# Optimization experiments

Measured on AMD Instinct MI355X. Metric: run time of the kernel, lower is better.

The kernel has to match this reference:

```python
import jax, jax.numpy as jnp
import numpy as np

IMAGE_SIZE = 128
FACES_PER_PIXEL = 4
BLUR_RADIUS = 0.01
EPS = 1e-8


def setup_inputs() -> dict:
    key = jax.random.key(0)
    k1, k2, k3 = jax.random.split(key, 3)
    B, V, F = 2, 2000, 800
    # verts are already projected to screen/NDC space: x,y in [-1,1], z > 0 (depth)
    xy = jax.random.uniform(k1, (B, V, 2), minval=-1.0, maxval=1.0)
    z = jax.random.uniform(k2, (B, V, 1), minval=0.5, maxval=2.5)
    verts = jnp.concatenate([xy, z], axis=-1).astype(jnp.float32)
    faces = jax.random.randint(k3, (F, 3), 0, V)
    return {"verts": verts, "faces": faces}


def _edge(a, b, p):
    # signed parallelogram area of (a -> b -> p), using xy components only
    return (p[..., 0] - a[..., 0]) * (b[..., 1] - a[..., 1]) - (
        p[..., 1] - a[..., 1]) * (b[..., 0] - a[..., 0])


def _seg_dist2(p, a, b):
    # squared distance from point p to segment [a, b] in 2D
    ab = b - a
    pa = p - a
    t = jnp.clip(jnp.sum(pa * ab, -1) / (jnp.sum(ab * ab, -1) + EPS), 0.0, 1.0)
    d = pa - t[..., None] * ab
    return jnp.sum(d * d, -1)


def _rasterize(verts, faces):
    H = W = IMAGE_SIZE
    K = FACES_PER_PIXEL
    B = verts.shape[0]
    fv = verts[:, faces]                      # [B,F,3,3] gather face vertices
    v0, v1, v2 = fv[:, :, 0], fv[:, :, 1], fv[:, :, 2]
    a0 = v0[:, None, :, :2]                   # [B,1,F,2]
    a1 = v1[:, None, :, :2]
    a2 = v2[:, None, :, :2]
    z0 = v0[:, None, :, 2]                    # [B,1,F]
    z1 = v1[:, None, :, 2]
    z2 = v2[:, None, :, 2]
    # pixel centers in NDC, pytorch3d convention: index 0 -> +1, last -> -1
    xs = 1.0 - 2.0 * (jnp.arange(W, dtype=verts.dtype) + 0.5) / W
    ys = 1.0 - 2.0 * (jnp.arange(H, dtype=verts.dtype) + 0.5) / H
    yy, xx = jnp.meshgrid(ys, xs, indexing="ij")
    p = jnp.stack([xx, yy], -1).reshape(1, -1, 1, 2)   # [1,P,1,2], P=H*W

    area = _edge(a0, a1, a2)                  # [B,1,F] signed face area*2
    w0 = _edge(a1, a2, p)                     # [B,P,F]
    w1 = _edge(a2, a0, p)
    w2 = _edge(a0, a1, p)
    denom = jnp.where(jnp.abs(area) > EPS, area,
                      jnp.where(area >= 0, EPS, -EPS))
    b0, b1, b2 = w0 / denom, w1 / denom, w2 / denom
    zpix = b0 * z0 + b1 * z1 + b2 * z2        # [B,P,F] interpolated depth

    inside = (b0 >= 0) & (b1 >= 0) & (b2 >= 0)
    dmin = jnp.minimum(_seg_dist2(p, a0, a1),
                       jnp.minimum(_seg_dist2(p, a1, a2),
                                   _seg_dist2(p, a2, a0)))
    dsign = jnp.where(inside, -dmin, dmin)    # signed squared edge distance

    valid = (inside | (dmin < BLUR_RADIUS)) & (zpix > EPS) & (
        jnp.abs(area) > EPS)
    zcand = jnp.where(valid, zpix, jnp.inf)
    _, idx = jax.lax.top_k(-zcand, K)         # K nearest faces per pixel

    take = lambda x: jnp.take_along_axis(x, idx, axis=-1)
    sel_valid = take(valid)
    pix_to_face = jnp.where(sel_valid, idx, -1)
    zbuf = jnp.where(sel_valid, take(zpix), -1.0)
    bary = jnp.stack([b0, b1, b2], -1)        # [B,P,F,3]
    bsel = jnp.take_along_axis(bary, idx[..., None], axis=2)  # [B,P,K,3]
    bsel = jnp.where(sel_valid[..., None], bsel, -1.0)
    dsel = jnp.where(sel_valid, take(dsign), -1.0)

    return (pix_to_face.reshape(B, H, W, K),
            zbuf.reshape(B, H, W, K),
            bsel.reshape(B, H, W, K, 3),
            dsel.reshape(B, H, W, K))


def reference(verts, faces):
    # Fragments: (pix_to_face, zbuf, bary_coords, dists)
    return _rasterize(verts, faces)
```

## Files before the change

kernel.cpp:

```cpp
#include <hip/hip_runtime.h>

#define IMG   128
#define KF    4
#define NF    800
#define NV    2000
#define NB    2
#define EPSF  1e-8f
#define BLURF 0.01f
#define CULL_D2 0.0103f
#define HEXT    0.0547f

typedef unsigned long long u64;
#define INVK ((((u64)0x7f800000u) << 32) | 0xffffffffu)

#pragma clang fp contract(off)

__device__ __forceinline__ float rcp2(float d) {
    float y = __builtin_amdgcn_rcpf(d);
    float e = __builtin_fmaf(-d, y, 1.0f);
    y = __builtin_fmaf(y, e, y);
    e = __builtin_fmaf(-d, y, 1.0f);
    y = __builtin_fmaf(y, e, y);
    return y;
}
__device__ __forceinline__ float fdivr(float n, float d, float y) {
    float q0 = n * y;
    float r  = __builtin_fmaf(-d, q0, n);
    return __builtin_fmaf(r, y, q0);
}

__device__ __forceinline__ float seg_d2(float pax, float pay, float abx, float aby) {
#pragma clang fp contract(off)
    float dd = (abx * abx + aby * aby) + EPSF;
    float t  = (pax * abx + pay * aby) / dd;
    t = fminf(fmaxf(t, 0.0f), 1.0f);
    float dx = pax - t * abx;
    float dy = pay - t * aby;
    return dx * dx + dy * dy;
}

__device__ __forceinline__ float seg_d2f(float pax, float pay, float abx, float aby) {
#pragma clang fp contract(off)
    float dd = (abx * abx + aby * aby) + EPSF;
    float n  = pax * abx + pay * aby;
    float t  = fdivr(n, dd, rcp2(dd));
    t = fminf(fmaxf(t, 0.0f), 1.0f);
    float dx = pax - t * abx;
    float dy = pay - t * aby;
    return dx * dx + dy * dy;
}

__device__ __forceinline__ void ins4(u64& s0, u64& s1, u64& s2, u64& s3, u64 k) {
    bool c0 = k < s0, c1 = k < s1, c2 = k < s2, c3 = k < s3;
    s3 = c2 ? s2 : (c3 ? k : s3);
    s2 = c1 ? s1 : (c2 ? k : s2);
    s1 = c0 ? s0 : (c1 ? k : s1);
    s0 = c0 ? k  : s0;
}

__global__ __launch_bounds__(256) void raster_p1(
    const float* __restrict__ verts,
    const int*   __restrict__ faces,
    u64* __restrict__ ws,
    int sh)
{
#pragma clang fp contract(off)
    extern __shared__ char dynLDS[];
    __shared__ u64 sK[2 * 4 * 64];
    __shared__ int sTot;

    const int S     = 1 << sh;
    const int chunk = NF >> sh;
    float* sFD  = (float*)dynLDS;
    int*   sList = (int*)(dynLDS + (size_t)chunk * 10 * sizeof(float));

    const int tid   = threadIdx.x;
    const int blk   = blockIdx.x;
    const int tile  = blk >> sh;
    const int slice = blk & (S - 1);
    const int b     = tile >> 8;
    const int trow  = (tile & 255) >> 4;
    const int tcol  = tile & 15;
    const float* vb = verts + b * NV * 3;
    const int fbase = slice * chunk;

    if (tid == 0) sTot = 0;

    for (int j = tid; j < chunk; j += 256) {
        int f = fbase + j;
        int i0 = faces[3 * f + 0], i1 = faces[3 * f + 1], i2 = faces[3 * f + 2];
        float a0x = vb[3 * i0], a0y = vb[3 * i0 + 1], z0 = vb[3 * i0 + 2];
        float a1x = vb[3 * i1], a1y = vb[3 * i1 + 1], z1 = vb[3 * i1 + 2];
        float a2x = vb[3 * i2], a2y = vb[3 * i2 + 1], z2 = vb[3 * i2 + 2];
        float area = (a2x - a0x) * (a1y - a0y) - (a2y - a0y) * (a1x - a0x);
        float aab  = fabsf(area);
        float denom = (aab > EPSF) ? area : (area >= 0.0f ? EPSF : -EPSF);
        float* fd = &sFD[j * 10];
        fd[0] = a0x; fd[1] = a0y; fd[2] = a1x; fd[3] = a1y; fd[4] = a2x; fd[5] = a2y;
        fd[6] = z0;  fd[7] = z1;  fd[8] = z2;  fd[9] = denom;
    }
    __syncthreads();

    const int wave = tid >> 6;
    const int lane = tid & 63;
    const int pr = lane >> 3, pc = lane & 7;
    const int row = trow * 8 + pr, col = tcol * 8 + pc;
    const float px = 1.0f - (2.0f * ((float)col + 0.5f)) / 128.0f;
    const float py = 1.0f - (2.0f * ((float)row + 0.5f)) / 128.0f;
    const float txmax = 1.0f - (2.0f * ((float)(tcol * 8)     + 0.5f)) / 128.0f;
    const float txmin = 1.0f - (2.0f * ((float)(tcol * 8 + 7) + 0.5f)) / 128.0f;
    const float tymax = 1.0f - (2.0f * ((float)(trow * 8)     + 0.5f)) / 128.0f;
    const float tymin = 1.0f - (2.0f * ((float)(trow * 8 + 7) + 0.5f)) / 128.0f;
    const float cx = 0.5f * (txmin + txmax);
    const float cy = 0.5f * (tymin + tymax);

    for (int j = tid; j < chunk; j += 256) {
        const float* fd = &sFD[j * 10];
        float a0x = fd[0], a0y = fd[1], a1x = fd[2], a1y = fd[3], a2x = fd[4], a2y = fd[5];
        float area = (a2x - a0x) * (a1y - a0y) - (a2y - a0y) * (a1x - a0x);
        bool surv = fabsf(area) > EPSF;
        float bxmin = fminf(a0x, fminf(a1x, a2x)) - 0.101f;
        float bxmax = fmaxf(a0x, fmaxf(a1x, a2x)) + 0.101f;
        float bymin = fminf(a0y, fminf(a1y, a2y)) - 0.101f;
        float bymax = fmaxf(a0y, fmaxf(a1y, a2y)) + 0.101f;
        surv &= !(bxmin > txmax || bxmax < txmin || bymin > tymax || bymax < tymin);
        float s = (area >= 0.0f) ? 1.0f : -1.0f;
        float e0x = a2x - a1x, e0y = a2y - a1y;
        float e1x = a0x - a2x, e1y = a0y - a2y;
        float e2x = a1x - a0x, e2y = a1y - a0y;
        float w0 = s * ((cx - a1x) * e0y - (cy - a1y) * e0x) + HEXT * (fabsf(e0x) + fabsf(e0y));
        float w1 = s * ((cx - a2x) * e1y - (cy - a2y) * e1x) + HEXT * (fabsf(e1x) + fabsf(e1y));
        float w2 = s * ((cx - a0x) * e2y - (cy - a0y) * e2x) + HEXT * (fabsf(e2x) + fabsf(e2y));
        float l0 = e0x * e0x + e0y * e0y;
        float l1 = e1x * e1x + e1y * e1y;
        float l2 = e2x * e2x + e2y * e2y;
        surv &= !((w0 < 0.0f) & (w0 * w0 > CULL_D2 * l0));
        surv &= !((w1 < 0.0f) & (w1 * w1 > CULL_D2 * l1));
        surv &= !((w2 < 0.0f) & (w2 * w2 > CULL_D2 * l2));
        if (surv) {
            int pos = atomicAdd(&sTot, 1);
            sList[pos] = j;
        }
    }
    __syncthreads();
    const int total = sTot;

    u64 s0 = INVK, s1 = INVK, s2 = INVK, s3 = INVK;
    for (int j = wave; j < total; j += 4) {
        int lf = sList[j];
        const float* fd = &sFD[lf * 10];
        float a0x = fd[0], a0y = fd[1], a1x = fd[2], a1y = fd[3], a2x = fd[4], a2y = fd[5];
        float z0 = fd[6], z1 = fd[7], z2 = fd[8], denom = fd[9];
        float e0x = a2x - a1x, e0y = a2y - a1y;
        float e1x = a0x - a2x, e1y = a0y - a2y;
        float e2x = a1x - a0x, e2y = a1y - a0y;
        float p0x = px - a0x, p0y = py - a0y;
        float p1x = px - a1x, p1y = py - a1y;
        float p2x = px - a2x, p2y = py - a2y;
        float w0 = p1x * e0y - p1y * e0x;
        float w1 = p2x * e1y - p2y * e1x;
        float w2 = p0x * e2y - p0y * e2x;
        float yd = rcp2(denom);
        float b0 = fdivr(w0, denom, yd);
        float b1 = fdivr(w1, denom, yd);
        float b2 = fdivr(w2, denom, yd);
        float zpix = (b0 * z0 + b1 * z1) + b2 * z2;
        bool inside = fminf(b0, fminf(b1, b2)) >= 0.0f;
        bool valid;
        if (__all(inside)) {
            valid = (zpix > EPSF);
        } else {
            float dA = seg_d2f(p0x, p0y, e2x, e2y);
            float dB = seg_d2f(p1x, p1y, e0x, e0y);
            float dC = seg_d2f(p2x, p2y, e1x, e1y);
            float dmin = fminf(dA, fminf(dB, dC));
            valid = (inside | (dmin < BLURF)) & (zpix > EPSF);
        }
        u64 key = valid ? ((((u64)__float_as_uint(zpix)) << 32) | (unsigned)(fbase + lf)) : INVK;
        if (__any(key < s3)) ins4(s0, s1, s2, s3, key);
    }

    if (wave >= 2) {
        int r = wave - 2;
        sK[(r * 4 + 0) * 64 + lane] = s0;
        sK[(r * 4 + 1) * 64 + lane] = s1;
        sK[(r * 4 + 2) * 64 + lane] = s2;
        sK[(r * 4 + 3) * 64 + lane] = s3;
    }
    __syncthreads();
    if (wave < 2) {
        ins4(s0, s1, s2, s3, sK[(wave * 4 + 0) * 64 + lane]);
        ins4(s0, s1, s2, s3, sK[(wave * 4 + 1) * 64 + lane]);
        ins4(s0, s1, s2, s3, sK[(wave * 4 + 2) * 64 + lane]);
        ins4(s0, s1, s2, s3, sK[(wave * 4 + 3) * 64 + lane]);
    }
    __syncthreads();
    if (wave == 1) {
        sK[0 * 64 + lane] = s0;
        sK[1 * 64 + lane] = s1;
        sK[2 * 64 + lane] = s2;
        sK[3 * 64 + lane] = s3;
    }
    __syncthreads();
    if (wave == 0) {
        ins4(s0, s1, s2, s3, sK[0 * 64 + lane]);
        ins4(s0, s1, s2, s3, sK[1 * 64 + lane]);
        ins4(s0, s1, s2, s3, sK[2 * 64 + lane]);
        ins4(s0, s1, s2, s3, sK[3 * 64 + lane]);
        u64* wrow = ws + (size_t)blk * 256;
        wrow[0 * 64 + lane] = s0;
        wrow[1 * 64 + lane] = s1;
        wrow[2 * 64 + lane] = s2;
        wrow[3 * 64 + lane] = s3;
    }
}

__global__ __launch_bounds__(256) void raster_p2(
    const float* __restrict__ verts,
    const int*   __restrict__ faces,
    const u64* __restrict__ ws,
    int sh,
    float* __restrict__ out0, float* __restrict__ out1,
    float* __restrict__ out2, float* __restrict__ out3)
{
#pragma clang fp contract(off)
    __shared__ u64 sK[4 * 64];
    const int S    = 1 << sh;
    const int tid  = threadIdx.x;
    const int tile = blockIdx.x;
    const int b    = tile >> 8;
    const int trow = (tile & 255) >> 4;
    const int tcol = tile & 15;
    const float* vb = verts + b * NV * 3;

    if (tid < 64) {
        u64 s0 = INVK, s1 = INVK, s2 = INVK, s3 = INVK;
        const u64* base = ws + (size_t)tile * S * 256;
        for (int s = 0; s < S; ++s) {
            ins4(s0, s1, s2, s3, base[s * 256 + 0 * 64 + tid]);
            ins4(s0, s1, s2, s3, base[s * 256 + 1 * 64 + tid]);
            ins4(s0, s1, s2, s3, base[s * 256 + 2 * 64 + tid]);
            ins4(s0, s1, s2, s3, base[s * 256 + 3 * 64 + tid]);
        }
        sK[0 * 64 + tid] = s0;
        sK[1 * 64 + tid] = s1;
        sK[2 * 64 + tid] = s2;
        sK[3 * 64 + tid] = s3;
    }
    __syncthreads();

    int pix = tid >> 2, k = tid & 3;
    u64 key = sK[k * 64 + pix];
    int prow = pix >> 3, pcol = pix & 7;
    int grow = trow * 8 + prow, gcol = tcol * 8 + pcol;
    int p = (b * IMG + grow) * IMG + gcol;
    float qx = 1.0f - (2.0f * ((float)gcol + 0.5f)) / 128.0f;
    float qy = 1.0f - (2.0f * ((float)grow + 0.5f)) / 128.0f;
    float o0 = -1.0f, o1 = -1.0f, ob0 = -1.0f, ob1 = -1.0f, ob2 = -1.0f, o3 = -1.0f;
    if ((unsigned)(key >> 32) != 0x7f800000u) {
        int fi = (int)(unsigned)(key & 0xffffffffu);
        int i0 = faces[3 * fi + 0], i1 = faces[3 * fi + 1], i2 = faces[3 * fi + 2];
        float a0x = vb[3 * i0], a0y = vb[3 * i0 + 1], z0 = vb[3 * i0 + 2];
        float a1x = vb[3 * i1], a1y = vb[3 * i1 + 1], z1 = vb[3 * i1 + 2];
        float a2x = vb[3 * i2], a2y = vb[3 * i2 + 1], z2 = vb[3 * i2 + 2];
        float area = (a2x - a0x) * (a1y - a0y) - (a2y - a0y) * (a1x - a0x);
        float aab  = fabsf(area);
        float denom = (aab > EPSF) ? area : (area >= 0.0f ? EPSF : -EPSF);
        float e0x = a2x - a1x, e0y = a2y - a1y;
        float e1x = a0x - a2x, e1y = a0y - a2y;
        float e2x = a1x - a0x, e2y = a1y - a0y;
        float p0x = qx - a0x, p0y = qy - a0y;
        float p1x = qx - a1x, p1y = qy - a1y;
        float p2x = qx - a2x, p2y = qy - a2y;
        float w0 = p1x * e0y - p1y * e0x;
        float w1 = p2x * e1y - p2y * e1x;
        float w2 = p0x * e2y - p0y * e2x;
        float b0 = w0 / denom, b1 = w1 / denom, b2 = w2 / denom;
        float zpix = (b0 * z0 + b1 * z1) + b2 * z2;
        bool inside = (b0 >= 0.0f) & (b1 >= 0.0f) & (b2 >= 0.0f);
        float dA = seg_d2(p0x, p0y, e2x, e2y);
        float dB = seg_d2(p1x, p1y, e0x, e0y);
        float dC = seg_d2(p2x, p2y, e1x, e1y);
        float dmin = fminf(dA, fminf(dB, dC));
        o0 = (float)fi;
        o1 = zpix;
        ob0 = b0; ob1 = b1; ob2 = b2;
        o3 = inside ? -dmin : dmin;
    }
    int o = p * KF + k;
    out0[o] = o0;
    out1[o] = o1;
    out2[o * 3 + 0] = ob0;
    out2[o * 3 + 1] = ob1;
    out2[o * 3 + 2] = ob2;
    out3[o] = o3;
}

extern "C" void kernel_launch(void* const* d_in, const int* in_sizes, int n_in,
                              void* d_out, int out_size, void* d_ws, size_t ws_size,
                              hipStream_t stream) {
    const float* verts = (const float*)d_in[0];
    const int*   faces = (const int*)d_in[1];
    float* out = (float*)d_out;
    const int n0 = NB * IMG * IMG * KF;

    const size_t per_slice = 512ull * 256 * sizeof(u64);
    int sh;
    if      (ws_size >= 4 * per_slice) sh = 2;
    else if (ws_size >= 2 * per_slice) sh = 1;
    else                               sh = 0;
    const int S = 1 << sh;
    const int chunk = NF >> sh;
    const size_t dyn = (size_t)chunk * 10 * sizeof(float) + (size_t)chunk * sizeof(int);

    raster_p1<<<dim3(512 * S), dim3(256), dyn, stream>>>(verts, faces, (u64*)d_ws, sh);
    raster_p2<<<dim3(512), dim3(256), 0, stream>>>(verts, faces, (const u64*)d_ws, sh,
        out,
        out + n0,
        out + 2 * n0,
        out + 5 * n0);
}
```

Measured before the change: 86.37 us.

## Fuse the two raster passes with a last-block merge and precompute per-face reciprocals

Result: slower. 174.6 us (+102.2%).

```diff
diff --git a/kernel.cpp b/kernel.cpp
--- a/kernel.cpp
+++ b/kernel.cpp
@@ -39,11 +39,11 @@
     return dx * dx + dy * dy;
 }
 
-__device__ __forceinline__ float seg_d2f(float pax, float pay, float abx, float aby) {
+__device__ __forceinline__ float seg_d2y(float pax, float pay, float abx, float aby, float y) {
 #pragma clang fp contract(off)
     float dd = (abx * abx + aby * aby) + EPSF;
     float n  = pax * abx + pay * aby;
-    float t  = fdivr(n, dd, rcp2(dd));
+    float t  = fdivr(n, dd, y);
     t = fminf(fmaxf(t, 0.0f), 1.0f);
     float dx = pax - t * abx;
     float dy = pay - t * aby;
@@ -58,21 +58,25 @@
     s0 = c0 ? k  : s0;
 }
 
-__global__ __launch_bounds__(256) void raster_p1(
+__global__ __launch_bounds__(256) void raster_fused(
     const float* __restrict__ verts,
     const int*   __restrict__ faces,
     u64* __restrict__ ws,
-    int sh)
+    int* __restrict__ cnt,
+    int sh,
+    float* __restrict__ out0, float* __restrict__ out1,
+    float* __restrict__ out2, float* __restrict__ out3)
 {
 #pragma clang fp contract(off)
     extern __shared__ char dynLDS[];
     __shared__ u64 sK[2 * 4 * 64];
     __shared__ int sTot;
+    __shared__ int sLast;
 
     const int S     = 1 << sh;
     const int chunk = NF >> sh;
     float* sFD  = (float*)dynLDS;
-    int*   sList = (int*)(dynLDS + (size_t)chunk * 10 * sizeof(float));
+    int*   sList = (int*)(dynLDS + (size_t)chunk * 14 * sizeof(float));
 
     const int tid   = threadIdx.x;
     const int blk   = blockIdx.x;
@@ -95,7 +99,7 @@
         float area = (a2x - a0x) * (a1y - a0y) - (a2y - a0y) * (a1x - a0x);
         float aab  = fabsf(area);
         float denom = (aab > EPSF) ? area : (area >= 0.0f ? EPSF : -EPSF);
-        float* fd = &sFD[j * 10];
+        float* fd = &sFD[j * 14];
         fd[0] = a0x; fd[1] = a0y; fd[2] = a1x; fd[3] = a1y; fd[4] = a2x; fd[5] = a2y;
         fd[6] = z0;  fd[7] = z1;  fd[8] = z2;  fd[9] = denom;
     }
@@ -115,7 +119,7 @@
     const float cy = 0.5f * (tymin + tymax);
 
     for (int j = tid; j < chunk; j += 256) {
-        const float* fd = &sFD[j * 10];
+        const float* fd = &sFD[j * 14];
         float a0x = fd[0], a0y = fd[1], a1x = fd[2], a1y = fd[3], a2x = fd[4], a2y = fd[5];
         float area = (a2x - a0x) * (a1y - a0y) - (a2y - a0y) * (a1x - a0x);
         bool surv = fabsf(area) > EPSF;
@@ -140,6 +144,11 @@
         if (surv) {
             int pos = atomicAdd(&sTot, 1);
             sList[pos] = j;
+            float* fdw = &sFD[j * 14];
+            fdw[10] = rcp2(area);
+            fdw[11] = rcp2(l2 + EPSF);
+            fdw[12] = rcp2(l0 + EPSF);
+            fdw[13] = rcp2(l1 + EPSF);
         }
     }
     __syncthreads();
@@ -148,9 +157,10 @@
     u64 s0 = INVK, s1 = INVK, s2 = INVK, s3 = INVK;
     for (int j = wave; j < total; j += 4) {
         int lf = sList[j];
-        const float* fd = &sFD[lf * 10];
+        const float* fd = &sFD[lf * 14];
         float a0x = fd[0], a0y = fd[1], a1x = fd[2], a1y = fd[3], a2x = fd[4], a2y = fd[5];
         float z0 = fd[6], z1 = fd[7], z2 = fd[8], denom = fd[9];
+        float yd = fd[10];
         float e0x = a2x - a1x, e0y = a2y - a1y;
         float e1x = a0x - a2x, e1y = a0y - a2y;
         float e2x = a1x - a0x, e2y = a1y - a0y;
@@ -160,7 +170,6 @@
         float w0 = p1x * e0y - p1y * e0x;
         float w1 = p2x * e1y - p2y * e1x;
         float w2 = p0x * e2y - p0y * e2x;
-        float yd = rcp2(denom);
         float b0 = fdivr(w0, denom, yd);
         float b1 = fdivr(w1, denom, yd);
         float b2 = fdivr(w2, denom, yd);
@@ -170,9 +179,9 @@
         if (__all(inside)) {
             valid = (zpix > EPSF);
         } else {
-            float dA = seg_d2f(p0x, p0y, e2x, e2y);
-            float dB = seg_d2f(p1x, p1y, e0x, e0y);
-            float dC = seg_d2f(p2x, p2y, e1x, e1y);
+            float dA = seg_d2y(p0x, p0y, e2x, e2y, fd[11]);
+            float dB = seg_d2y(p1x, p1y, e0x, e0y, fd[12]);
+            float dC = seg_d2y(p2x, p2y, e1x, e1y, fd[13]);
             float dmin = fminf(dA, fminf(dB, dC));
             valid = (inside | (dmin < BLURF)) & (zpix > EPSF);
         }
@@ -213,30 +222,21 @@
         wrow[2 * 64 + lane] = s2;
         wrow[3 * 64 + lane] = s3;
     }
-}
-
-__global__ __launch_bounds__(256) void raster_p2(
-    const float* __restrict__ verts,
-    const int*   __restrict__ faces,
-    const u64* __restrict__ ws,
-    int sh,
-    float* __restrict__ out0, float* __restrict__ out1,
-    float* __restrict__ out2, float* __restrict__ out3)
-{
-#pragma clang fp contract(off)
-    __shared__ u64 sK[4 * 64];
-    const int S    = 1 << sh;
-    const int tid  = threadIdx.x;
-    const int tile = blockIdx.x;
-    const int b    = tile >> 8;
-    const int trow = (tile & 255) >> 4;
-    const int tcol = tile & 15;
-    const float* vb = verts + b * NV * 3;
+
+    __syncthreads();
+    if (tid == 0) {
+        __threadfence();
+        int old = atomicAdd(&cnt[tile], 1);
+        sLast = (old == S - 1) ? 1 : 0;
+    }
+    __syncthreads();
+    if (!sLast) return;
+    __threadfence();
 
     if (tid < 64) {
-        u64 s0 = INVK, s1 = INVK, s2 = INVK, s3 = INVK;
-        const u64* base = ws + (size_t)tile * S * 256;
+        const u64* base = ws + (size_t)(tile * S) * 256;
         for (int s = 0; s < S; ++s) {
+            if (s == slice) continue;
             ins4(s0, s1, s2, s3, base[s * 256 + 0 * 64 + tid]);
             ins4(s0, s1, s2, s3, base[s * 256 + 1 * 64 + tid]);
             ins4(s0, s1, s2, s3, base[s * 256 + 2 * 64 + tid]);
@@ -306,15 +306,20 @@
 
     const size_t per_slice = 512ull * 256 * sizeof(u64);
     int sh;
-    if      (ws_size >= 4 * per_slice) sh = 2;
-    else if (ws_size >= 2 * per_slice) sh = 1;
-    else                               sh = 0;
+    if      (ws_size >= 4 * per_slice + 4096) sh = 2;
+    else if (ws_size >= 2 * per_slice + 4096) sh = 1;
+    else                                      sh = 0;
     const int S = 1 << sh;
     const int chunk = NF >> sh;
-    const size_t dyn = (size_t)chunk * 10 * sizeof(float) + (size_t)chunk * sizeof(int);
-
-    raster_p1<<<dim3(512 * S), dim3(256), dyn, stream>>>(verts, faces, (u64*)d_ws, sh);
-    raster_p2<<<dim3(512), dim3(256), 0, stream>>>(verts, faces, (const u64*)d_ws, sh,
+    const size_t dyn = (size_t)chunk * 14 * sizeof(float) + (size_t)chunk * sizeof(int);
+
+    const size_t partials = 512ull * S * 256 * sizeof(u64);
+    int* cnt = (int*)((char*)d_ws + partials);
+
+    hipMemsetAsync(cnt, 0, 512 * sizeof(int), stream);
+
+    raster_fused<<<dim3(512 * S), dim3(256), dyn, stream>>>(
+        verts, faces, (u64*)d_ws, cnt, sh,
         out,
         out + n0,
         out + 2 * n0,
```
